# Kernel tuning notes

Measured on AMD Instinct MI355X. Metric: run time of the kernel, lower is better.

## Reference

```python
import jax, jax.numpy as jnp
import numpy as np
from jax import lax

EPS = 1e-5

def _conv(x, w, b):
    # sign-binarized conv: sign(x) conv sign(w) + float bias; 3x3, pad 1, NCHW
    y = lax.conv_general_dilated(jnp.sign(x), jnp.sign(w), (1, 1), ((1, 1), (1, 1)),
                                 dimension_numbers=("NCHW", "OIHW", "NCHW"))
    return y + b[None, :, None, None]

def _bn(x, g, beta, mean, var):
    # eval-mode batchnorm with running stats
    inv = g / jnp.sqrt(var + EPS)
    return x * inv[None, :, None, None] + (beta - mean * inv)[None, :, None, None]

def _pool2(x):
    return lax.reduce_window(x, -jnp.inf, lax.max, (1, 1, 2, 2), (1, 1, 2, 2), "VALID")

def setup_inputs() -> dict:
    key = jax.random.key(0)
    ks = jax.random.split(key, 16)
    B, num_classes = 4096, 2
    x = jax.random.normal(ks[0], (B, 1, 64, 64), dtype=jnp.float32)
    def conv_params(k, cout, cin):
        k1, k2 = jax.random.split(k)
        w = jax.random.normal(k1, (cout, cin, 3, 3), dtype=jnp.float32) * 0.1
        b = jax.random.normal(k2, (cout,), dtype=jnp.float32) * 0.01
        return w, b
    def bn_params(k, c):
        k1, k2, k3 = jax.random.split(k, 3)
        g = 1.0 + 0.1 * jax.random.normal(k1, (c,), dtype=jnp.float32)
        beta = 0.1 * jax.random.normal(k2, (c,), dtype=jnp.float32)
        mean = 0.1 * jax.random.normal(k3, (c,), dtype=jnp.float32)
        var = jnp.ones((c,), dtype=jnp.float32)
        return g, beta, mean, var
    w1, b1 = conv_params(ks[1], 8, 1)
    w2, b2 = conv_params(ks[2], 16, 8)
    w3, b3 = conv_params(ks[3], 32, 16)
    g1, be1, m1, v1 = bn_params(ks[4], 8)
    g2, be2, m2, v2 = bn_params(ks[5], 16)
    g3, be3, m3, v3 = bn_params(ks[6], 32)
    fc_w = jax.random.normal(ks[7], (num_classes, 32 * 8 * 8), dtype=jnp.float32) * 0.02
    fc_b = jnp.zeros((num_classes,), dtype=jnp.float32)
    return dict(x=x, w1=w1, b1=b1, g1=g1, be1=be1, m1=m1, v1=v1,
                w2=w2, b2=b2, g2=g2, be2=be2, m2=m2, v2=v2,
                w3=w3, b3=b3, g3=g3, be3=be3, m3=m3, v3=v3,
                fc_w=fc_w, fc_b=fc_b)

def reference(x, w1, b1, g1, be1, m1, v1,
              w2, b2, g2, be2, m2, v2,
              w3, b3, g3, be3, m3, v3, fc_w, fc_b):
    h = _pool2(jax.nn.relu(_bn(_conv(x, w1, b1), g1, be1, m1, v1)))   # [B,8,32,32]
    h = _pool2(jax.nn.relu(_bn(_conv(h, w2, b2), g2, be2, m2, v2)))   # [B,16,16,16]
    h = _pool2(jax.nn.relu(_bn(_conv(h, w3, b3), g3, be3, m3, v3)))   # [B,32,8,8]
    h = h.reshape(h.shape[0], -1)                                      # [B,2048]
    logits = h @ fc_w.T + fc_b
    return jax.nn.softmax(logits, axis=1)
```

## Files before the change

kernel.cpp:

```cpp
#include <hip/hip_runtime.h>
#include <stdint.h>

#define EPS 1e-5f
typedef unsigned long long u64;
typedef unsigned int u32;
typedef unsigned short u16;
typedef unsigned char u8;

struct Consts {
  u32 p2r[16][4];
  u64 q3m0[32];
  u64 q3m1[32];
  u32 q3m2[32];
  int lo2[16];
  u32 rng2[16];
  float inv3[32];
  float A3[32];
  float b3v[32];
  float fcb[2];
  u8  lut[9 * 512];
};
static_assert(sizeof(Consts) == 6024, "layout");

__global__ void prep_kernel(
    const float* __restrict__ w1, const float* __restrict__ b1,
    const float* __restrict__ g1, const float* __restrict__ be1,
    const float* __restrict__ m1, const float* __restrict__ v1,
    const float* __restrict__ w2, const float* __restrict__ b2,
    const float* __restrict__ g2, const float* __restrict__ be2,
    const float* __restrict__ m2, const float* __restrict__ v2,
    const float* __restrict__ w3, const float* __restrict__ b3,
    const float* __restrict__ g3, const float* __restrict__ be3,
    const float* __restrict__ m3, const float* __restrict__ v3,
    const float* __restrict__ fcb, Consts* __restrict__ out)
{
  int tid = threadIdx.x;

  if (blockIdx.x == 0) {
    if (tid < 16) {
      int c = tid;
      u32 rm[3] = {0u, 0u, 0u};
      for (int ci = 0; ci < 8; ++ci)
        for (int t = 0; t < 9; ++t) {
          float w = w2[(c * 8 + ci) * 9 + t];
          if (w > 0.f) rm[t / 3] |= 1u << ((t % 3) * 8 + ci);
        }
      out->p2r[c][0] = rm[0]; out->p2r[c][1] = rm[1];
      out->p2r[c][2] = rm[2]; out->p2r[c][3] = 0u;
      float inv = __fdiv_rn(g2[c], __fsqrt_rn(__fadd_rn(v2[c], EPS)));
      float A   = __fsub_rn(be2[c], __fmul_rn(m2[c], inv));
      int lo = 1000, hi = -1000;
      for (int s = -72; s <= 72; ++s) {
        float y  = __fadd_rn((float)s, b2[c]);
        float bn = __fadd_rn(__fmul_rn(y, inv), A);
        if (bn > 0.f) { if (s < lo) lo = s; if (s > hi) hi = s; }
      }
      out->lo2[c] = lo; out->rng2[c] = (u32)(hi - lo);
    }
    if (tid < 32) {
      int c = tid;
      u64 q0 = 0, q1 = 0; u32 q2 = 0;
      for (int ci = 0; ci < 16; ++ci)
        for (int t = 0; t < 9; ++t) {
          float w = w3[(c * 16 + ci) * 9 + t];
          if (w > 0.f) {
            if (t < 4)      q0 |= 1ull << (t * 16 + ci);
            else if (t < 8) q1 |= 1ull << ((t - 4) * 16 + ci);
            else            q2 |= 1u << ci;
          }
        }
      out->q3m0[c] = q0; out->q3m1[c] = q1; out->q3m2[c] = q2;
      float inv = __fdiv_rn(g3[c], __fsqrt_rn(__fadd_rn(v3[c], EPS)));
      out->inv3[c] = inv;
      out->A3[c]   = __fsub_rn(be3[c], __fmul_rn(m3[c], inv));
      out->b3v[c]  = b3[c];
    }
    if (tid < 2) out->fcb[tid] = fcb[tid];
    return;
  }

  __shared__ float inv1s[8], A1s[8];
  __shared__ int   sw1[8][9];
  if (tid < 8) {
    int c = tid;
    float inv = __fdiv_rn(g1[c], __fsqrt_rn(__fadd_rn(v1[c], EPS)));
    inv1s[c] = inv;
    A1s[c]   = __fsub_rn(be1[c], __fmul_rn(m1[c], inv));
    for (int t = 0; t < 9; ++t) sw1[c][t] = (w1[c * 9 + t] > 0.f) ? 1 : -1;
  }
  __syncthreads();
  int e = (blockIdx.x - 1) * 256 + tid;
  int type = e >> 9, pat = e & 511;
  int ty = type / 3, tx = type % 3;
  u8 byte = 0;
  for (int c = 0; c < 8; ++c) {
    int s = 0;
    for (int t = 0; t < 9; ++t) {
      int dr = t / 3, dc = t % 3;
      bool valid = !((ty == 0 && dr == 0) || (ty == 2 && dr == 2) ||
                     (tx == 0 && dc == 0) || (tx == 2 && dc == 2));
      if (!valid) continue;
      s += ((pat >> t) & 1) ? sw1[c][t] : -sw1[c][t];
    }
    float y  = __fadd_rn((float)s, b1[c]);
    float bn = __fadd_rn(__fmul_rn(y, inv1s[c]), A1s[c]);
    if (bn > 0.f) byte |= (u8)(1u << c);
  }
  out->lut[e] = byte;
}

__launch_bounds__(256, 4)
__global__ void main_kernel(const float* __restrict__ x, const float* __restrict__ fcw,
                            const Consts* __restrict__ cs, float* __restrict__ out, int B)
{
  __shared__ __align__(16) u8  slut[9 * 512];
  __shared__ __align__(16) u64 xb[2][64];
  __shared__ __align__(16) u8  s2p[2][34][36];
  __shared__ __align__(16) u16 s3p[2][18][18];
  __shared__ float red[2][2][2];

  const int tid = threadIdx.x;
  const int wv = tid >> 6, lane = tid & 63;
  const int im = wv >> 1, w = wv & 1;
  const int img = blockIdx.x * 2 + im;

  for (int i = tid; i < 1152; i += 256) ((u32*)slut)[i] = ((const u32*)cs->lut)[i];
  for (int i = tid; i < 612; i += 256) ((u32*)s2p)[i] = 0;
  for (int i = tid; i < 324; i += 256) ((u32*)s3p)[i] = 0;

  if (img < B) {
    const float* xp = x + (size_t)img * 4096 + (size_t)w * 2048;
    float xv[32];
    #pragma unroll
    for (int rr = 0; rr < 32; ++rr) xv[rr] = xp[rr * 64 + lane];
    u64 my = 0;
    #pragma unroll
    for (int rr = 0; rr < 32; ++rr) {
      u64 m = __ballot(xv[rr] > 0.f);
      if (lane == rr) my = m;
    }
    if (lane < 32) xb[im][w * 32 + lane] = my;
  }
  __syncthreads();

  {
    const int c = lane & 31, h = lane >> 5;
    const int j0 = 2 * c;
    const u32 sa0  = (c == 0) ? 0u : (u32)(j0 - 1);
    const u32 msk0 = (c == 0) ? 3u : 7u;
    const u32 sft0 = (c == 0) ? 1u : 0u;
    const u32 base0 = ((c == 0) ? 0u : 1u) << 9;
    const u32 base1 = ((c == 31) ? 2u : 1u) << 9;
    #pragma unroll
    for (int p = 0; p < 8; ++p) {
      const int pr = w * 16 + h * 8 + p;
      const int i0 = 2 * pr;
      u64 r0 = (i0 > 0) ? xb[im][i0 - 1] : 0ull;
      u64 r1 = xb[im][i0];
      u64 r2 = xb[im][i0 + 1];
      u64 r3 = (i0 + 2 < 64) ? xb[im][i0 + 2] : 0ull;
      u32 acc = 0;
      #pragma unroll
      for (int a = 0; a < 2; ++a) {
        u64 ra = a ? r1 : r0, rb = a ? r2 : r1, rc = a ? r3 : r2;
        const int i = i0 + a;
        const u32 ti9 = ((i == 0) ? 0u : ((i == 63) ? 6u : 3u)) << 9;
        u32 ea = ((u32)(ra >> sa0) & msk0) << sft0;
        u32 eb = ((u32)(rb >> sa0) & msk0) << sft0;
        u32 ec = ((u32)(rc >> sa0) & msk0) << sft0;
        acc |= slut[ti9 + base0 + (ea | (eb << 3) | (ec << 6))];
        u32 fa = (u32)(ra >> j0) & 7u;
        u32 fb = (u32)(rb >> j0) & 7u;
        u32 fc = (u32)(rc >> j0) & 7u;
        acc |= slut[ti9 + base1 + (fa | (fb << 3) | (fc << 6))];
      }
      s2p[im][pr + 1][c + 1] = (u8)acc;
    }
  }
  __syncthreads();

  float fw0[16], fw1[16];
  #pragma unroll
  for (int cc = 0; cc < 16; ++cc) {
    const int f = ((16 * w + cc) << 6) + lane;
    fw0[cc] = fcw[f];
    fw1[cc] = fcw[2048 + f];
  }

  {
    const int idx = w * 64 + lane;
    const int pi = idx >> 3, pjp = idx & 7;
    const int bo = 4 * pjp;
    const u32* rp0 = (const u32*)&s2p[im][2 * pi + 0][bo];
    const u32* rp1 = (const u32*)&s2p[im][2 * pi + 1][bo];
    const u32* rp2 = (const u32*)&s2p[im][2 * pi + 2][bo];
    const u32* rp3 = (const u32*)&s2p[im][2 * pi + 3][bo];
    u32 rl[4], rh[4];
    rl[0] = rp0[0]; rh[0] = rp0[1];
    rl[1] = rp1[0]; rh[1] = rp1[1];
    rl[2] = rp2[0]; rh[2] = rp2[1];
    rl[3] = rp3[0]; rh[3] = rp3[1];

    u32 d0[8], d1[8], d2[8]; int pc[8]; u32 cw[8];
    #pragma unroll
    for (int k = 0; k < 8; ++k) {
      const int o = k >> 2, a = (k >> 1) & 1, bb = k & 1;
      const int sh = 8 * (2 * o + bb);
      d0[k] = __builtin_amdgcn_alignbit(rh[a],     rl[a],     sh) & 0xFFFFFFu;
      d1[k] = __builtin_amdgcn_alignbit(rh[a + 1], rl[a + 1], sh) & 0xFFFFFFu;
      d2[k] = __builtin_amdgcn_alignbit(rh[a + 2], rl[a + 2], sh) & 0xFFFFFFu;
      pc[k] = __popc(d0[k]) + __popc(d1[k]) + __popc(d2[k]);
      cw[k] = 0u;
    }

    #pragma unroll 1
    for (int ch = 15; ch >= 0; --ch) {
      const u32 m0 = cs->p2r[ch][0];
      const u32 m1 = cs->p2r[ch][1];
      const u32 m2 = cs->p2r[ch][2];
      const int nlo = -cs->lo2[ch];
      const u32 rng = cs->rng2[ch];
      #pragma unroll
      for (int k = 0; k < 8; ++k) {
        int ps = __popc(d0[k] & m0) + __popc(d1[k] & m1) + __popc(d2[k] & m2);
        u32 t = (u32)(2 * ps - pc[k] + nlo);
        cw[k] = cw[k] + cw[k] + ((t <= rng) ? 1u : 0u);
      }
    }
    s3p[im][pi + 1][2 * pjp + 1] = (u16)(cw[0] | cw[1] | cw[2] | cw[3]);
    s3p[im][pi + 1][2 * pjp + 2] = (u16)(cw[4] | cw[5] | cw[6] | cw[7]);
  }
  __syncthreads();

  float l0 = 0.f, l1 = 0.f;
  {
    const int pi = lane >> 3, pj = lane & 7;
    const u32* p0 = (const u32*)(&s3p[im][2 * pi + 0][2 * pj]);
    const u32* p1 = (const u32*)(&s3p[im][2 * pi + 1][2 * pj]);
    const u32* p2 = (const u32*)(&s3p[im][2 * pi + 2][2 * pj]);
    const u32* p3 = (const u32*)(&s3p[im][2 * pi + 3][2 * pj]);
    const u64 rr0 = (u64)p0[0] | ((u64)p0[1] << 32);
    const u64 rr1 = (u64)p1[0] | ((u64)p1[1] << 32);
    const u64 rr2 = (u64)p2[0] | ((u64)p2[1] << 32);
    const u64 rr3 = (u64)p3[0] | ((u64)p3[1] << 32);

    u64 q0a, q1a, q0b, q1b, q0c, q1c, q0d, q1d;
    u32 q2a, q2b, q2c, q2d;
    int pca, pcb, pcc, pcd;
    {
      u64 ta, tb, tc;
      ta = rr0;       tb = rr1;       tc = rr2;
      q0a = (ta & 0xFFFFFFFFFFFFull) | ((tb & 0xFFFFull) << 48);
      q1a = ((tb >> 16) & 0xFFFFFFFFull) | ((tc & 0xFFFFFFFFull) << 32);
      q2a = (u32)((tc >> 32) & 0xFFFFull);
      pca = __popcll(q0a) + __popcll(q1a) + __popc(q2a);
      ta = rr0 >> 16; tb = rr1 >> 16; tc = rr2 >> 16;
      q0b = (ta & 0xFFFFFFFFFFFFull) | ((tb & 0xFFFFull) << 48);
      q1b = ((tb >> 16) & 0xFFFFFFFFull) | ((tc & 0xFFFFFFFFull) << 32);
      q2b = (u32)((tc >> 32) & 0xFFFFull);
      pcb = __popcll(q0b) + __popcll(q1b) + __popc(q2b);
      ta = rr1;       tb = rr2;       tc = rr3;
      q0c = (ta & 0xFFFFFFFFFFFFull) | ((tb & 0xFFFFull) << 48);
      q1c = ((tb >> 16) & 0xFFFFFFFFull) | ((tc & 0xFFFFFFFFull) << 32);
      q2c = (u32)((tc >> 32) & 0xFFFFull);
      pcc = __popcll(q0c) + __popcll(q1c) + __popc(q2c);
      ta = rr1 >> 16; tb = rr2 >> 16; tc = rr3 >> 16;
      q0d = (ta & 0xFFFFFFFFFFFFull) | ((tb & 0xFFFFull) << 48);
      q1d = ((tb >> 16) & 0xFFFFFFFFull) | ((tc & 0xFFFFFFFFull) << 32);
      q2d = (u32)((tc >> 32) & 0xFFFFull);
      pcd = __popcll(q0d) + __popcll(q1d) + __popc(q2d);
    }

    #pragma unroll 2
    for (int cc = 0; cc < 16; ++cc) {
      const int c = 16 * w + cc;
      const u64 m0 = cs->q3m0[c], m1 = cs->q3m1[c];
      const u32 m2 = cs->q3m2[c];
      int t0 = 2 * (__popcll(q0a & m0) + __popcll(q1a & m1) + __popc(q2a & m2)) - pca;
      int t1 = 2 * (__popcll(q0b & m0) + __popcll(q1b & m1) + __popc(q2b & m2)) - pcb;
      int t2 = 2 * (__popcll(q0c & m0) + __popcll(q1c & m1) + __popc(q2c & m2)) - pcc;
      int t3 = 2 * (__popcll(q0d & m0) + __popcll(q1d & m1) + __popc(q2d & m2)) - pcd;
      int smax = max(max(t0, t1), max(t2, t3));
      int smin = min(min(t0, t1), min(t2, t3));
      float inv = cs->inv3[c];
      int sel = (inv > 0.f) ? smax : smin;
      float y   = __fadd_rn((float)sel, cs->b3v[c]);
      float bn  = __fadd_rn(__fmul_rn(y, inv), cs->A3[c]);
      float val = fmaxf(bn, 0.f);
      l0 = fmaf(val, fw0[cc], l0);
      l1 = fmaf(val, fw1[cc], l1);
    }
  }

  #pragma unroll
  for (int d = 32; d >= 1; d >>= 1) {
    l0 += __shfl_xor(l0, d, 64);
    l1 += __shfl_xor(l1, d, 64);
  }
  if (lane == 0) { red[im][w][0] = l0; red[im][w][1] = l1; }
  __syncthreads();
  if ((tid & 127) == 0 && img < B) {
    float a0 = red[im][0][0] + red[im][1][0] + cs->fcb[0];
    float a1 = red[im][0][1] + red[im][1][1] + cs->fcb[1];
    float mm = fmaxf(a0, a1);
    float e0 = expf(a0 - mm), e1 = expf(a1 - mm);
    float sden = e0 + e1;
    out[(size_t)img * 2]     = e0 / sden;
    out[(size_t)img * 2 + 1] = e1 / sden;
  }
}

extern "C" void kernel_launch(void* const* d_in, const int* in_sizes, int n_in,
                              void* d_out, int out_size, void* d_ws, size_t ws_size,
                              hipStream_t stream) {
  const float* x   = (const float*)d_in[0];
  const float* w1  = (const float*)d_in[1];
  const float* b1  = (const float*)d_in[2];
  const float* g1  = (const float*)d_in[3];
  const float* be1 = (const float*)d_in[4];
  const float* m1  = (const float*)d_in[5];
  const float* v1  = (const float*)d_in[6];
  const float* w2  = (const float*)d_in[7];
  const float* b2  = (const float*)d_in[8];
  const float* g2  = (const float*)d_in[9];
  const float* be2 = (const float*)d_in[10];
  const float* m2  = (const float*)d_in[11];
  const float* v2  = (const float*)d_in[12];
  const float* w3  = (const float*)d_in[13];
  const float* b3  = (const float*)d_in[14];
  const float* g3  = (const float*)d_in[15];
  const float* be3 = (const float*)d_in[16];
  const float* m3  = (const float*)d_in[17];
  const float* v3  = (const float*)d_in[18];
  const float* fcw = (const float*)d_in[19];
  const float* fcb = (const float*)d_in[20];

  int B = in_sizes[0] / 4096;
  Consts* cs = (Consts*)d_ws;

  prep_kernel<<<19, 256, 0, stream>>>(w1, b1, g1, be1, m1, v1,
                                      w2, b2, g2, be2, m2, v2,
                                      w3, b3, g3, be3, m3, v3, fcb, cs);
  int nblk = (B + 1) / 2;
  main_kernel<<<nblk, 256, 0, stream>>>(x, fcw, cs, (float*)d_out, B);
}
```

Before: 65.23 us.

## Process two images per wave pair to amortize per-block setup and constant loads

New measurement: 70.08 us. +7.4%, slower.

```diff
diff --git a/kernel.cpp b/kernel.cpp
--- a/kernel.cpp
+++ b/kernel.cpp
@@ -109,38 +109,44 @@
   out->lut[e] = byte;
 }
 
-__launch_bounds__(256, 4)
+__launch_bounds__(256, 3)
 __global__ void main_kernel(const float* __restrict__ x, const float* __restrict__ fcw,
                             const Consts* __restrict__ cs, float* __restrict__ out, int B)
 {
   __shared__ __align__(16) u8  slut[9 * 512];
-  __shared__ __align__(16) u64 xb[2][64];
-  __shared__ __align__(16) u8  s2p[2][34][36];
-  __shared__ __align__(16) u16 s3p[2][18][18];
-  __shared__ float red[2][2][2];
+  __shared__ __align__(16) u64 xb[4][64];
+  __shared__ __align__(16) u8  s2p[4][34][36];
+  __shared__ __align__(16) u16 s3p[4][18][18];
+  __shared__ float red[4][2][2];
 
   const int tid = threadIdx.x;
   const int wv = tid >> 6, lane = tid & 63;
-  const int im = wv >> 1, w = wv & 1;
-  const int img = blockIdx.x * 2 + im;
+  const int pp = wv >> 1, w = wv & 1;
+  const int sA = 2 * pp, sB = sA + 1;
+  const int imgA = blockIdx.x * 4 + sA;
+  const int imgB = imgA + 1;
 
   for (int i = tid; i < 1152; i += 256) ((u32*)slut)[i] = ((const u32*)cs->lut)[i];
-  for (int i = tid; i < 612; i += 256) ((u32*)s2p)[i] = 0;
-  for (int i = tid; i < 324; i += 256) ((u32*)s3p)[i] = 0;
-
-  if (img < B) {
-    const float* xp = x + (size_t)img * 4096 + (size_t)w * 2048;
-    float xv[32];
-    #pragma unroll
-    for (int rr = 0; rr < 32; ++rr) xv[rr] = xp[rr * 64 + lane];
-    u64 my = 0;
-    #pragma unroll
-    for (int rr = 0; rr < 32; ++rr) {
-      u64 m = __ballot(xv[rr] > 0.f);
-      if (lane == rr) my = m;
-    }
-    if (lane < 32) xb[im][w * 32 + lane] = my;
-  }
+  for (int i = tid; i < 1224; i += 256) ((u32*)s2p)[i] = 0;
+  for (int i = tid; i < 648;  i += 256) ((u32*)s3p)[i] = 0;
+
+  auto stageA = [&](int slot, int img) {
+    if (img < B) {
+      const float* xp = x + (size_t)img * 4096 + (size_t)w * 2048;
+      float xv[32];
+      #pragma unroll
+      for (int rr = 0; rr < 32; ++rr) xv[rr] = xp[rr * 64 + lane];
+      u64 my = 0;
+      #pragma unroll
+      for (int rr = 0; rr < 32; ++rr) {
+        u64 m = __ballot(xv[rr] > 0.f);
+        if (lane == rr) my = m;
+      }
+      if (lane < 32) xb[slot][w * 32 + lane] = my;
+    }
+  };
+  stageA(sA, imgA);
+  stageA(sB, imgB);
   __syncthreads();
 
   {
@@ -151,31 +157,35 @@
     const u32 sft0 = (c == 0) ? 1u : 0u;
     const u32 base0 = ((c == 0) ? 0u : 1u) << 9;
     const u32 base1 = ((c == 31) ? 2u : 1u) << 9;
-    #pragma unroll
-    for (int p = 0; p < 8; ++p) {
-      const int pr = w * 16 + h * 8 + p;
-      const int i0 = 2 * pr;
-      u64 r0 = (i0 > 0) ? xb[im][i0 - 1] : 0ull;
-      u64 r1 = xb[im][i0];
-      u64 r2 = xb[im][i0 + 1];
-      u64 r3 = (i0 + 2 < 64) ? xb[im][i0 + 2] : 0ull;
-      u32 acc = 0;
-      #pragma unroll
-      for (int a = 0; a < 2; ++a) {
-        u64 ra = a ? r1 : r0, rb = a ? r2 : r1, rc = a ? r3 : r2;
-        const int i = i0 + a;
-        const u32 ti9 = ((i == 0) ? 0u : ((i == 63) ? 6u : 3u)) << 9;
-        u32 ea = ((u32)(ra >> sa0) & msk0) << sft0;
-        u32 eb = ((u32)(rb >> sa0) & msk0) << sft0;
-        u32 ec = ((u32)(rc >> sa0) & msk0) << sft0;
-        acc |= slut[ti9 + base0 + (ea | (eb << 3) | (ec << 6))];
-        u32 fa = (u32)(ra >> j0) & 7u;
-        u32 fb = (u32)(rb >> j0) & 7u;
-        u32 fc = (u32)(rc >> j0) & 7u;
-        acc |= slut[ti9 + base1 + (fa | (fb << 3) | (fc << 6))];
-      }
-      s2p[im][pr + 1][c + 1] = (u8)acc;
-    }
+    auto stageB = [&](int slot) {
+      #pragma unroll
+      for (int p = 0; p < 8; ++p) {
+        const int pr = w * 16 + h * 8 + p;
+        const int i0 = 2 * pr;
+        u64 r0 = (i0 > 0) ? xb[slot][i0 - 1] : 0ull;
+        u64 r1 = xb[slot][i0];
+        u64 r2 = xb[slot][i0 + 1];
+        u64 r3 = (i0 + 2 < 64) ? xb[slot][i0 + 2] : 0ull;
+        u32 acc = 0;
+        #pragma unroll
+        for (int a = 0; a < 2; ++a) {
+          u64 ra = a ? r1 : r0, rb = a ? r2 : r1, rc = a ? r3 : r2;
+          const int i = i0 + a;
+          const u32 ti9 = ((i == 0) ? 0u : ((i == 63) ? 6u : 3u)) << 9;
+          u32 ea = ((u32)(ra >> sa0) & msk0) << sft0;
+          u32 eb = ((u32)(rb >> sa0) & msk0) << sft0;
+          u32 ec = ((u32)(rc >> sa0) & msk0) << sft0;
+          acc |= slut[ti9 + base0 + (ea | (eb << 3) | (ec << 6))];
+          u32 fa = (u32)(ra >> j0) & 7u;
+          u32 fb = (u32)(rb >> j0) & 7u;
+          u32 fc = (u32)(rc >> j0) & 7u;
+          acc |= slut[ti9 + base1 + (fa | (fb << 3) | (fc << 6))];
+        }
+        s2p[slot][pr + 1][c + 1] = (u8)acc;
+      }
+    };
+    stageB(sA);
+    stageB(sB);
   }
   __syncthreads();
 
@@ -191,26 +201,31 @@
     const int idx = w * 64 + lane;
     const int pi = idx >> 3, pjp = idx & 7;
     const int bo = 4 * pjp;
-    const u32* rp0 = (const u32*)&s2p[im][2 * pi + 0][bo];
-    const u32* rp1 = (const u32*)&s2p[im][2 * pi + 1][bo];
-    const u32* rp2 = (const u32*)&s2p[im][2 * pi + 2][bo];
-    const u32* rp3 = (const u32*)&s2p[im][2 * pi + 3][bo];
-    u32 rl[4], rh[4];
-    rl[0] = rp0[0]; rh[0] = rp0[1];
-    rl[1] = rp1[0]; rh[1] = rp1[1];
-    rl[2] = rp2[0]; rh[2] = rp2[1];
-    rl[3] = rp3[0]; rh[3] = rp3[1];
-
-    u32 d0[8], d1[8], d2[8]; int pc[8]; u32 cw[8];
+    u32 rlA[4], rhA[4], rlB[4], rhB[4];
+    #pragma unroll
+    for (int r = 0; r < 4; ++r) {
+      const u32* ra = (const u32*)&s2p[sA][2 * pi + r][bo];
+      const u32* rb = (const u32*)&s2p[sB][2 * pi + r][bo];
+      rlA[r] = ra[0]; rhA[r] = ra[1];
+      rlB[r] = rb[0]; rhB[r] = rb[1];
+    }
+
+    u32 d0A[8], d1A[8], d2A[8], cwA[8]; int pcA[8];
+    u32 d0B[8], d1B[8], d2B[8], cwB[8]; int pcB[8];
     #pragma unroll
     for (int k = 0; k < 8; ++k) {
       const int o = k >> 2, a = (k >> 1) & 1, bb = k & 1;
       const int sh = 8 * (2 * o + bb);
-      d0[k] = __builtin_amdgcn_alignbit(rh[a],     rl[a],     sh) & 0xFFFFFFu;
-      d1[k] = __builtin_amdgcn_alignbit(rh[a + 1], rl[a + 1], sh) & 0xFFFFFFu;
-      d2[k] = __builtin_amdgcn_alignbit(rh[a + 2], rl[a + 2], sh) & 0xFFFFFFu;
-      pc[k] = __popc(d0[k]) + __popc(d1[k]) + __popc(d2[k]);
-      cw[k] = 0u;
+      d0A[k] = __builtin_amdgcn_alignbit(rhA[a],     rlA[a],     sh) & 0xFFFFFFu;
+      d1A[k] = __builtin_amdgcn_alignbit(rhA[a + 1], rlA[a + 1], sh) & 0xFFFFFFu;
+      d2A[k] = __builtin_amdgcn_alignbit(rhA[a + 2], rlA[a + 2], sh) & 0xFFFFFFu;
+      pcA[k] = __popc(d0A[k]) + __popc(d1A[k]) + __popc(d2A[k]);
+      cwA[k] = 0u;
+      d0B[k] = __builtin_amdgcn_alignbit(rhB[a],     rlB[a],     sh) & 0xFFFFFFu;
+      d1B[k] = __builtin_amdgcn_alignbit(rhB[a + 1], rlB[a + 1], sh) & 0xFFFFFFu;
+      d2B[k] = __builtin_amdgcn_alignbit(rhB[a + 2], rlB[a + 2], sh) & 0xFFFFFFu;
+      pcB[k] = __popc(d0B[k]) + __popc(d1B[k]) + __popc(d2B[k]);
+      cwB[k] = 0u;
     }
 
     #pragma unroll 1
@@ -222,91 +237,117 @@
       const u32 rng = cs->rng2[ch];
       #pragma unroll
       for (int k = 0; k < 8; ++k) {
-        int ps = __popc(d0[k] & m0) + __popc(d1[k] & m1) + __popc(d2[k] & m2);
-        u32 t = (u32)(2 * ps - pc[k] + nlo);
-        cw[k] = cw[k] + cw[k] + ((t <= rng) ? 1u : 0u);
-      }
-    }
-    s3p[im][pi + 1][2 * pjp + 1] = (u16)(cw[0] | cw[1] | cw[2] | cw[3]);
-    s3p[im][pi + 1][2 * pjp + 2] = (u16)(cw[4] | cw[5] | cw[6] | cw[7]);
-  }
-  __syncthreads();
-
-  float l0 = 0.f, l1 = 0.f;
+        int psA = __popc(d0A[k] & m0) + __popc(d1A[k] & m1) + __popc(d2A[k] & m2);
+        u32 tA = (u32)(2 * psA - pcA[k] + nlo);
+        cwA[k] = cwA[k] + cwA[k] + ((tA <= rng) ? 1u : 0u);
+        int psB = __popc(d0B[k] & m0) + __popc(d1B[k] & m1) + __popc(d2B[k] & m2);
+        u32 tB = (u32)(2 * psB - pcB[k] + nlo);
+        cwB[k] = cwB[k] + cwB[k] + ((tB <= rng) ? 1u : 0u);
+      }
+    }
+    s3p[sA][pi + 1][2 * pjp + 1] = (u16)(cwA[0] | cwA[1] | cwA[2] | cwA[3]);
+    s3p[sA][pi + 1][2 * pjp + 2] = (u16)(cwA[4] | cwA[5] | cwA[6] | cwA[7]);
+    s3p[sB][pi + 1][2 * pjp + 1] = (u16)(cwB[0] | cwB[1] | cwB[2] | cwB[3]);
+    s3p[sB][pi + 1][2 * pjp + 2] = (u16)(cwB[4] | cwB[5] | cwB[6] | cwB[7]);
+  }
+  __syncthreads();
+
+  float l0A = 0.f, l1A = 0.f, l0B = 0.f, l1B = 0.f;
   {
     const int pi = lane >> 3, pj = lane & 7;
-    const u32* p0 = (const u32*)(&s3p[im][2 * pi + 0][2 * pj]);
-    const u32* p1 = (const u32*)(&s3p[im][2 * pi + 1][2 * pj]);
-    const u32* p2 = (const u32*)(&s3p[im][2 * pi + 2][2 * pj]);
-    const u32* p3 = (const u32*)(&s3p[im][2 * pi + 3][2 * pj]);
-    const u64 rr0 = (u64)p0[0] | ((u64)p0[1] << 32);
-    const u64 rr1 = (u64)p1[0] | ((u64)p1[1] << 32);
-    const u64 rr2 = (u64)p2[0] | ((u64)p2[1] << 32);
-    const u64 rr3 = (u64)p3[0] | ((u64)p3[1] << 32);
-
-    u64 q0a, q1a, q0b, q1b, q0c, q1c, q0d, q1d;
-    u32 q2a, q2b, q2c, q2d;
-    int pca, pcb, pcc, pcd;
-    {
-      u64 ta, tb, tc;
-      ta = rr0;       tb = rr1;       tc = rr2;
-      q0a = (ta & 0xFFFFFFFFFFFFull) | ((tb & 0xFFFFull) << 48);
-      q1a = ((tb >> 16) & 0xFFFFFFFFull) | ((tc & 0xFFFFFFFFull) << 32);
-      q2a = (u32)((tc >> 32) & 0xFFFFull);
-      pca = __popcll(q0a) + __popcll(q1a) + __popc(q2a);
-      ta = rr0 >> 16; tb = rr1 >> 16; tc = rr2 >> 16;
-      q0b = (ta & 0xFFFFFFFFFFFFull) | ((tb & 0xFFFFull) << 48);
-      q1b = ((tb >> 16) & 0xFFFFFFFFull) | ((tc & 0xFFFFFFFFull) << 32);
-      q2b = (u32)((tc >> 32) & 0xFFFFull);
-      pcb = __popcll(q0b) + __popcll(q1b) + __popc(q2b);
-      ta = rr1;       tb = rr2;       tc = rr3;
-      q0c = (ta & 0xFFFFFFFFFFFFull) | ((tb & 0xFFFFull) << 48);
-      q1c = ((tb >> 16) & 0xFFFFFFFFull) | ((tc & 0xFFFFFFFFull) << 32);
-      q2c = (u32)((tc >> 32) & 0xFFFFull);
-      pcc = __popcll(q0c) + __popcll(q1c) + __popc(q2c);
-      ta = rr1 >> 16; tb = rr2 >> 16; tc = rr3 >> 16;
-      q0d = (ta & 0xFFFFFFFFFFFFull) | ((tb & 0xFFFFull) << 48);
-      q1d = ((tb >> 16) & 0xFFFFFFFFull) | ((tc & 0xFFFFFFFFull) << 32);
-      q2d = (u32)((tc >> 32) & 0xFFFFull);
-      pcd = __popcll(q0d) + __popcll(q1d) + __popc(q2d);
-    }
+
+    u64 q0A[4], q1A[4]; u32 q2A[4]; int pcA[4];
+    u64 q0B[4], q1B[4]; u32 q2B[4]; int pcB[4];
+    auto loadwin = [&](int slot, u64 (&q0)[4], u64 (&q1)[4], u32 (&q2)[4], int (&pc)[4]) {
+      const u32* p0 = (const u32*)(&s3p[slot][2 * pi + 0][2 * pj]);
+      const u32* p1 = (const u32*)(&s3p[slot][2 * pi + 1][2 * pj]);
+      const u32* p2 = (const u32*)(&s3p[slot][2 * pi + 2][2 * pj]);
+      const u32* p3 = (const u32*)(&s3p[slot][2 * pi + 3][2 * pj]);
+      const u64 rr0 = (u64)p0[0] | ((u64)p0[1] << 32);
+      const u64 rr1 = (u64)p1[0] | ((u64)p1[1] << 32);
+      const u64 rr2 = (u64)p2[0] | ((u64)p2[1] << 32);
+      const u64 rr3 = (u64)p3[0] | ((u64)p3[1] << 32);
+      #pragma unroll
+      for (int a = 0; a < 2; ++a) {
+        u64 wa = a ? rr1 : rr0, wb = a ? rr2 : rr1, wc = a ? rr3 : rr2;
+        #pragma unroll
+        for (int b = 0; b < 2; ++b) {
+          const int sidx = a * 2 + b;
+          u64 ta = wa >> (16 * b), tb = wb >> (16 * b), tc = wc >> (16 * b);
+          q0[sidx] = (ta & 0xFFFFFFFFFFFFull) | ((tb & 0xFFFFull) << 48);
+          q1[sidx] = ((tb >> 16) & 0xFFFFFFFFull) | ((tc & 0xFFFFFFFFull) << 32);
+          q2[sidx] = (u32)((tc >> 32) & 0xFFFFull);
+          pc[sidx] = __popcll(q0[sidx]) + __popcll(q1[sidx]) + __popc(q2[sidx]);
+        }
+      }
+    };
+    loadwin(sA, q0A, q1A, q2A, pcA);
+    loadwin(sB, q0B, q1B, q2B, pcB);
 
     #pragma unroll 2
     for (int cc = 0; cc < 16; ++cc) {
       const int c = 16 * w + cc;
       const u64 m0 = cs->q3m0[c], m1 = cs->q3m1[c];
       const u32 m2 = cs->q3m2[c];
-      int t0 = 2 * (__popcll(q0a & m0) + __popcll(q1a & m1) + __popc(q2a & m2)) - pca;
-      int t1 = 2 * (__popcll(q0b & m0) + __popcll(q1b & m1) + __popc(q2b & m2)) - pcb;
-      int t2 = 2 * (__popcll(q0c & m0) + __popcll(q1c & m1) + __popc(q2c & m2)) - pcc;
-      int t3 = 2 * (__popcll(q0d & m0) + __popcll(q1d & m1) + __popc(q2d & m2)) - pcd;
-      int smax = max(max(t0, t1), max(t2, t3));
-      int smin = min(min(t0, t1), min(t2, t3));
-      float inv = cs->inv3[c];
-      int sel = (inv > 0.f) ? smax : smin;
-      float y   = __fadd_rn((float)sel, cs->b3v[c]);
-      float bn  = __fadd_rn(__fmul_rn(y, inv), cs->A3[c]);
-      float val = fmaxf(bn, 0.f);
-      l0 = fmaf(val, fw0[cc], l0);
-      l1 = fmaf(val, fw1[cc], l1);
+      const float inv = cs->inv3[c];
+      const float bv  = cs->b3v[c];
+      const float A3v = cs->A3[c];
+
+      int t0 = 2 * (__popcll(q0A[0] & m0) + __popcll(q1A[0] & m1) + __popc(q2A[0] & m2)) - pcA[0];
+      int t1 = 2 * (__popcll(q0A[1] & m0) + __popcll(q1A[1] & m1) + __popc(q2A[1] & m2)) - pcA[1];
+      int t2 = 2 * (__popcll(q0A[2] & m0) + __popcll(q1A[2] & m1) + __popc(q2A[2] & m2)) - pcA[2];
+      int t3 = 2 * (__popcll(q0A[3] & m0) + __popcll(q1A[3] & m1) + __popc(q2A[3] & m2)) - pcA[3];
+      int u0 = 2 * (__popcll(q0B[0] & m0) + __popcll(q1B[0] & m1) + __popc(q2B[0] & m2)) - pcB[0];
+      int u1 = 2 * (__popcll(q0B[1] & m0) + __popcll(q1B[1] & m1) + __popc(q2B[1] & m2)) - pcB[1];
+      int u2 = 2 * (__popcll(q0B[2] & m0) + __popcll(q1B[2] & m1) + __popc(q2B[2] & m2)) - pcB[2];
+      int u3 = 2 * (__popcll(q0B[3] & m0) + __popcll(q1B[3] & m1) + __popc(q2B[3] & m2)) - pcB[3];
+
+      int smaxA = max(max(t0, t1), max(t2, t3));
+      int sminA = min(min(t0, t1), min(t2, t3));
+      int smaxB = max(max(u0, u1), max(u2, u3));
+      int sminB = min(min(u0, u1), min(u2, u3));
+      int selA = (inv > 0.f) ? smaxA : sminA;
+      int selB = (inv > 0.f) ? smaxB : sminB;
+      float yA  = __fadd_rn((float)selA, bv);
+      float yB  = __fadd_rn((float)selB, bv);
+      float bnA = __fadd_rn(__fmul_rn(yA, inv), A3v);
+      float bnB = __fadd_rn(__fmul_rn(yB, inv), A3v);
+      float vA  = fmaxf(bnA, 0.f);
+      float vB  = fmaxf(bnB, 0.f);
+      l0A = fmaf(vA, fw0[cc], l0A);
+      l1A = fmaf(vA, fw1[cc], l1A);
+      l0B = fmaf(vB, fw0[cc], l0B);
+      l1B = fmaf(vB, fw1[cc], l1B);
     }
   }
 
   #pragma unroll
   for (int d = 32; d >= 1; d >>= 1) {
-    l0 += __shfl_xor(l0, d, 64);
-    l1 += __shfl_xor(l1, d, 64);
-  }
-  if (lane == 0) { red[im][w][0] = l0; red[im][w][1] = l1; }
-  __syncthreads();
-  if ((tid & 127) == 0 && img < B) {
-    float a0 = red[im][0][0] + red[im][1][0] + cs->fcb[0];
-    float a1 = red[im][0][1] + red[im][1][1] + cs->fcb[1];
-    float mm = fmaxf(a0, a1);
-    float e0 = expf(a0 - mm), e1 = expf(a1 - mm);
-    float sden = e0 + e1;
-    out[(size_t)img * 2]     = e0 / sden;
-    out[(size_t)img * 2 + 1] = e1 / sden;
+    l0A += __shfl_xor(l0A, d, 64);
+    l1A += __shfl_xor(l1A, d, 64);
+    l0B += __shfl_xor(l0B, d, 64);
+    l1B += __shfl_xor(l1B, d, 64);
+  }
+  if (lane == 0) {
+    red[sA][w][0] = l0A; red[sA][w][1] = l1A;
+    red[sB][w][0] = l0B; red[sB][w][1] = l1B;
+  }
+  __syncthreads();
+  if (w == 0 && lane == 0) {
+    #pragma unroll
+    for (int s = 0; s < 2; ++s) {
+      const int slot = sA + s;
+      const int img = blockIdx.x * 4 + slot;
+      if (img < B) {
+        float a0 = red[slot][0][0] + red[slot][1][0] + cs->fcb[0];
+        float a1 = red[slot][0][1] + red[slot][1][1] + cs->fcb[1];
+        float mm = fmaxf(a0, a1);
+        float e0 = expf(a0 - mm), e1 = expf(a1 - mm);
+        float sden = e0 + e1;
+        out[(size_t)img * 2]     = e0 / sden;
+        out[(size_t)img * 2 + 1] = e1 / sden;
+      }
+    }
   }
 }
 
@@ -341,6 +382,6 @@
   prep_kernel<<<19, 256, 0, stream>>>(w1, b1, g1, be1, m1, v1,
                                       w2, b2, g2, be2, m2, v2,
                                       w3, b3, g3, be3, m3, v3, fcb, cs);
-  int nblk = (B + 1) / 2;
+  int nblk = (B + 3) / 4;
   main_kernel<<<nblk, 256, 0, stream>>>(x, fcw, cs, (float*)d_out, B);
 }
```
